# Optimization experiments

Hardware: AMD Instinct MI355X
Metric: run time of the kernel (lower is better)

## Reference

```python
import jax, jax.numpy as jnp
import numpy as np

D_MODEL = 256
NHEAD = 8
HEAD_DIM = D_MODEL // NHEAD
NUM_BOND_TYPES = 5
SCALE = float(np.sqrt(HEAD_DIM))


def setup_inputs() -> dict:
    key = jax.random.key(0)
    ks = jax.random.split(key, 12)
    B, N = 8, 1024
    s = 1.0 / np.sqrt(D_MODEL)
    x = jax.random.normal(ks[0], (B, N, D_MODEL), dtype=jnp.float32)
    adj_matrix = jax.random.randint(ks[1], (B, N, N), 0, NUM_BOND_TYPES, dtype=jnp.int32)
    Wq = jax.random.uniform(ks[2], (D_MODEL, D_MODEL), jnp.float32, -s, s)
    bq = jax.random.uniform(ks[3], (D_MODEL,), jnp.float32, -s, s)
    Wk = jax.random.uniform(ks[4], (D_MODEL, D_MODEL), jnp.float32, -s, s)
    bk = jax.random.uniform(ks[5], (D_MODEL,), jnp.float32, -s, s)
    Wv = jax.random.uniform(ks[6], (D_MODEL, D_MODEL), jnp.float32, -s, s)
    bv = jax.random.uniform(ks[7], (D_MODEL,), jnp.float32, -s, s)
    Wo = jax.random.uniform(ks[8], (D_MODEL, D_MODEL), jnp.float32, -s, s)
    bo = jax.random.uniform(ks[9], (D_MODEL,), jnp.float32, -s, s)
    # edge bias table (num_bond_types, nhead); torch init is zeros, use small randn so it matters
    edge_emb = 0.02 * jax.random.normal(ks[10], (NUM_BOND_TYPES, NHEAD), dtype=jnp.float32)
    return {"x": x, "adj_matrix": adj_matrix, "Wq": Wq, "bq": bq, "Wk": Wk, "bk": bk,
            "Wv": Wv, "bv": bv, "Wo": Wo, "bo": bo, "edge_emb": edge_emb}


def reference(x, adj_matrix, Wq, bq, Wk, bk, Wv, bv, Wo, bo, edge_emb):
    B, N, _ = x.shape
    # projections -> (B, H, N, Dh)
    def proj(W, b):
        return (x @ W.T + b).reshape(B, N, NHEAD, HEAD_DIM).transpose(0, 2, 1, 3)
    Q = proj(Wq, bq)
    K = proj(Wk, bk)
    V = proj(Wv, bv)
    scores = jnp.einsum('bhqd,bhkd->bhqk', Q, K) / SCALE  # (B,H,N,N)
    bias = edge_emb[adj_matrix]                            # (B,N,N,H)
    scores = scores + bias.transpose(0, 3, 1, 2)
    attn = jax.nn.softmax(scores, axis=-1)                 # dropout p=0 (eval) -> identity
    out = jnp.einsum('bhqk,bhkd->bhqd', attn, V)
    out = out.transpose(0, 2, 1, 3).reshape(B, N, D_MODEL)
    return out @ Wo.T + bo
```

## Files before the change

kernel.cpp:

```cpp
#include <hip/hip_runtime.h>
#include <hip/hip_bf16.h>

typedef float f32x4 __attribute__((ext_vector_type(4)));
typedef float f32x16 __attribute__((ext_vector_type(16)));
typedef __bf16 bf16x8 __attribute__((ext_vector_type(8)));
typedef unsigned int uint2v __attribute__((ext_vector_type(2)));

#define MFMA16(a, b, c) __builtin_amdgcn_mfma_f32_16x16x32_bf16((a), (b), (c), 0, 0, 0)
#define MFMA32(a, b, c) __builtin_amdgcn_mfma_f32_32x32x16_bf16((a), (b), (c), 0, 0, 0)

static __device__ __forceinline__ short f2s(float f) {
    __hip_bfloat16 h = __float2bfloat16(f);
    return *reinterpret_cast<short*>(&h);
}
static __device__ __forceinline__ unsigned int cvtpk(float lo, float hi) {
    unsigned int r;
    asm("v_cvt_pk_bf16_f32 %0, %1, %2" : "=v"(r) : "v"(lo), "v"(hi));
    return r;
}
static __device__ __forceinline__ float exp2f_fast(float x) {
#if __has_builtin(__builtin_amdgcn_exp2f)
    return __builtin_amdgcn_exp2f(x);
#else
    return exp2f(x);
#endif
}

__global__ __launch_bounds__(256)
void qkv3_and_gather(const float* __restrict__ x,
                     const float* __restrict__ Wq, const float* __restrict__ bq,
                     const float* __restrict__ Wk, const float* __restrict__ bk,
                     const float* __restrict__ Wv, const float* __restrict__ bv,
                     short* __restrict__ Qb, short* __restrict__ Kb, short* __restrict__ Vb,
                     const int* __restrict__ adj, unsigned int* __restrict__ adjG)
{
    __shared__ short As[128 * 72];
    __shared__ short Bs[3][64 * 72];

    const int bx = blockIdx.x;
    const int tid = threadIdx.x;

    if (bx < 256) {
        const int lane = tid & 63;
        const int wid = tid >> 6;
        const int wr = wid >> 1, wc = wid & 1;
        const int g = lane >> 4, li = lane & 15;

        const int m0 = (bx & 63) * 128;
        const int wc0 = (bx >> 6) * 64;

        const float* Wm[3]  = { Wq, Wk, Wv };
        const float* bm[3]  = { bq, bk, bv };
        short*       Om[3]  = { Qb, Kb, Vb };

        f32x4 acc[3][4][2] = {};

        const int sr = tid >> 4;
        const int sc4 = (tid & 15) * 4;

        for (int k0 = 0; k0 < 256; k0 += 64) {
            __syncthreads();
#pragma unroll
            for (int it = 0; it < 8; ++it) {
                int row = sr + it * 16;
                float4 v = *reinterpret_cast<const float4*>(&x[(m0 + row) * 256 + k0 + sc4]);
                short4 s4;
                s4.x = f2s(v.x); s4.y = f2s(v.y); s4.z = f2s(v.z); s4.w = f2s(v.w);
                *reinterpret_cast<short4*>(&As[row * 72 + sc4]) = s4;
            }
#pragma unroll
            for (int mat = 0; mat < 3; ++mat) {
#pragma unroll
                for (int it = 0; it < 4; ++it) {
                    int row = sr + it * 16;
                    float4 v = *reinterpret_cast<const float4*>(
                        &Wm[mat][(wc0 + row) * 256 + k0 + sc4]);
                    short4 s4;
                    s4.x = f2s(v.x); s4.y = f2s(v.y); s4.z = f2s(v.z); s4.w = f2s(v.w);
                    *reinterpret_cast<short4*>(&Bs[mat][row * 72 + sc4]) = s4;
                }
            }
            __syncthreads();
#pragma unroll
            for (int ks = 0; ks < 2; ++ks) {
                const int kb = ks * 32 + g * 8;
                bf16x8 a[4];
#pragma unroll
                for (int i = 0; i < 4; ++i)
                    a[i] = *reinterpret_cast<const bf16x8*>(&As[(wr * 64 + i * 16 + li) * 72 + kb]);
#pragma unroll
                for (int mat = 0; mat < 3; ++mat) {
                    bf16x8 bfr[2];
#pragma unroll
                    for (int j = 0; j < 2; ++j)
                        bfr[j] = *reinterpret_cast<const bf16x8*>(
                            &Bs[mat][(wc * 32 + j * 16 + li) * 72 + kb]);
#pragma unroll
                    for (int i = 0; i < 4; ++i)
#pragma unroll
                        for (int j = 0; j < 2; ++j)
                            acc[mat][i][j] = MFMA16(a[i], bfr[j], acc[mat][i][j]);
                }
            }
        }

#pragma unroll
        for (int mat = 0; mat < 3; ++mat) {
#pragma unroll
            for (int j = 0; j < 2; ++j) {
                const int colW = wc0 + wc * 32 + j * 16 + li;
                const int h = colW >> 5, d = colW & 31;
                const float bv_ = bm[mat][colW];
#pragma unroll
                for (int i = 0; i < 4; ++i) {
#pragma unroll
                    for (int r = 0; r < 4; ++r) {
                        const int row = m0 + wr * 64 + i * 16 + g * 4 + r;
                        const int bb = row >> 10, nq = row & 1023;
                        Om[mat][((bb * 8 + h) * 1024 + nq) * 32 + d] =
                            f2s(acc[mat][i][j][r] + bv_);
                    }
                }
            }
        }
    } else {
        const int gx = bx - 256;
        const int qt = gx & 31;
        const int b  = (gx >> 5) & 7;
        const int j0 = (gx >> 8) * 8;

        const int4* base = reinterpret_cast<const int4*>(
            adj + ((size_t)(b * 1024 + qt * 32)) * 1024);
        unsigned int* outT = adjG + ((size_t)(b * 32 + qt)) * 16 * 512;

        const int t = tid >> 4;
        const int i = (tid >> 1) & 7;
        const int laneb = 32 * (tid & 1);

#pragma unroll
        for (int jj = 0; jj < 8; ++jj) {
            const int j = j0 + jj;
            const int4 c = base[j * 256 + tid];
            const unsigned int packed =
                (unsigned)c.x | ((unsigned)c.y << 8) | ((unsigned)c.z << 16) | ((unsigned)c.w << 24);
            outT[t * 512 + i * 64 + (j + laneb)] = packed;
        }
    }
}

__global__ __launch_bounds__(256, 2)
void attn11(const short* __restrict__ Qb, const short* __restrict__ Kb,
            const short* __restrict__ Vb, const unsigned int* __restrict__ adjG,
            const float* __restrict__ edge_emb, short* __restrict__ AO)
{
    __shared__ __align__(16) short Ks[4][64 * 36];
    __shared__ __align__(16) short Vt[4][32 * 72];
    __shared__ float Etab[8];

    const int tid = threadIdx.x, lane = tid & 63, wid = tid >> 6;
    const int l5 = lane & 31, h32 = lane >> 5;

    const int orig = blockIdx.x + blockIdx.y * 8;
    const int flat = (orig & 7) * 64 + (orig >> 3);
    const int qb = flat & 7, bh = flat >> 3;
    const int b = bh >> 3, h = bh & 7;
    const int qt = qb * 4 + wid;
    const int q  = qt * 32 + l5;

    const short* Qh = Qb + bh * (1024 * 32);
    const short* Kh = Kb + bh * (1024 * 32);
    const short* Vh = Vb + bh * (1024 * 32);
    const unsigned int* adjT = adjG + ((size_t)(b * 32 + qt)) * 16 * 512;

    if (tid < 5) Etab[tid] = __expf(edge_emb[tid * 8 + h]);

    const bf16x8 qf0 = *reinterpret_cast<const bf16x8*>(&Qh[q * 32 + h32 * 8]);
    const bf16x8 qf1 = *reinterpret_cast<const bf16x8*>(&Qh[q * 32 + 16 + h32 * 8]);

    const float c1 = 0.25503486f;
    const f32x16 zero16 = {};

    f32x16 o[2] = {};
    float lr[2] = { 0.f, 0.f };

    const int sr = tid >> 2;
    const int sc = (tid & 3) * 8;
    const int srh = sr >> 3, srl = sr & 7;
    const int scg2 = (sc >> 3) << 1;

#pragma unroll
    for (int par = 0; par < 2; ++par) {
        const int row = par * 64 + sr;
        int4 kr = *reinterpret_cast<const int4*>(&Kh[row * 32 + sc]);
        int4 vr = *reinterpret_cast<const int4*>(&Vh[row * 32 + sc]);
        short* kd = &Ks[par][sr * 36 + sc];
        *reinterpret_cast<short4*>(kd)     = *reinterpret_cast<short4*>(&kr);
        *reinterpret_cast<short4*>(kd + 4) = *(reinterpret_cast<short4*>(&kr) + 1);
        const short* vs = reinterpret_cast<const short*>(&vr);
#pragma unroll
        for (int i = 0; i < 8; ++i) {
            const int swz = srh ^ i ^ scg2;
            Vt[par][(sc + i) * 72 + swz * 8 + srl] = vs[i];
        }
    }
    __syncthreads();

    for (int p = 0; p < 8; ++p) {
        const int cur = (p & 1) * 2;

        unsigned int a4[2][8];
#pragma unroll
        for (int par = 0; par < 2; ++par)
#pragma unroll
            for (int i = 0; i < 8; ++i)
                a4[par][i] = adjT[(2 * p + par) * 512 + i * 64 + lane];

        int4 kn[2], vn[2];
        if (p < 7) {
#pragma unroll
            for (int par = 0; par < 2; ++par) {
                const int row = (p + 1) * 128 + par * 64 + sr;
                kn[par] = *reinterpret_cast<const int4*>(&Kh[row * 32 + sc]);
                vn[par] = *reinterpret_cast<const int4*>(&Vh[row * 32 + sc]);
            }
        }

        f32x16 s[2][2];
#pragma unroll
        for (int par = 0; par < 2; ++par)
#pragma unroll
            for (int ks = 0; ks < 2; ++ks) {
                union { short4 h4[2]; bf16x8 v; } kfa, kfb;
                const int rowb = (ks * 32 + l5) * 36;
                const short* KsC = &Ks[cur + par][0];
                kfa.h4[0] = *reinterpret_cast<const short4*>(&KsC[rowb + h32 * 8]);
                kfa.h4[1] = *reinterpret_cast<const short4*>(&KsC[rowb + h32 * 8 + 4]);
                kfb.h4[0] = *reinterpret_cast<const short4*>(&KsC[rowb + 16 + h32 * 8]);
                kfb.h4[1] = *reinterpret_cast<const short4*>(&KsC[rowb + 16 + h32 * 8 + 4]);
                s[par][ks] = MFMA32(kfa.v, qf0, zero16);
                s[par][ks] = MFMA32(kfb.v, qf1, s[par][ks]);
            }

        unsigned int pw[2][2][8];
#pragma unroll
        for (int par = 0; par < 2; ++par) {
            float lsum = 0.f;
#pragma unroll
            for (int ks = 0; ks < 2; ++ks) {
#pragma unroll
                for (int rg = 0; rg < 4; ++rg) {
                    const unsigned int aw4 = a4[par][ks * 4 + rg] << 2;
                    float pv[4];
#pragma unroll
                    for (int j = 0; j < 4; ++j) {
                        const float Ev = *reinterpret_cast<const float*>(
                            reinterpret_cast<const char*>(&Etab[0]) +
                            ((aw4 >> (8 * j)) & 0x3FCu));
                        const float pe = exp2f_fast(s[par][ks][rg * 4 + j] * c1);
                        const float pp = pe * Ev;
                        pv[j] = pp;
                        lsum += pp;
                    }
                    pw[par][ks][rg * 2 + 0] = cvtpk(pv[0], pv[1]);
                    pw[par][ks][rg * 2 + 1] = cvtpk(pv[2], pv[3]);
                }
            }
            lr[par] += lsum;
        }

#pragma unroll
        for (int par = 0; par < 2; ++par)
#pragma unroll
            for (int kc = 0; kc < 4; ++kc) {
                const int ks = kc >> 1, half = kc & 1;
                const unsigned int A0 = pw[par][ks][4 * half + 0], A1 = pw[par][ks][4 * half + 1];
                const unsigned int B0 = pw[par][ks][4 * half + 2], B1 = pw[par][ks][4 * half + 3];
                union { unsigned int u[4]; bf16x8 v; } P;
#if __has_builtin(__builtin_amdgcn_permlane32_swap)
                uint2v r02 = __builtin_amdgcn_permlane32_swap(A0, B0, false, false);
                uint2v r13 = __builtin_amdgcn_permlane32_swap(A1, B1, false, false);
                P.u[0] = r02.x; P.u[1] = r13.x;
                P.u[2] = r02.y; P.u[3] = r13.y;
#else
                const unsigned int send0 = h32 ? A0 : B0, send1 = h32 ? A1 : B1;
                const unsigned int rv0 = __shfl_xor(send0, 32);
                const unsigned int rv1 = __shfl_xor(send1, 32);
                const unsigned int own0 = h32 ? B0 : A0, own1 = h32 ? B1 : A1;
                P.u[0] = h32 ? rv0 : own0;
                P.u[1] = h32 ? rv1 : own1;
                P.u[2] = h32 ? own0 : rv0;
                P.u[3] = h32 ? own1 : rv1;
#endif
                const int swzr = (kc * 2 + h32) ^ (l5 & 7) ^ ((l5 >> 3) << 1);
                bf16x8 vf = *reinterpret_cast<const bf16x8*>(
                    &Vt[cur + par][l5 * 72 + swzr * 8]);
                o[par] = MFMA32(vf, P.v, o[par]);
            }

        if (p < 7) {
#pragma unroll
            for (int par = 0; par < 2; ++par) {
                short* kd = &Ks[(cur ^ 2) + par][sr * 36 + sc];
                *reinterpret_cast<short4*>(kd)     = *reinterpret_cast<short4*>(&kn[par]);
                *reinterpret_cast<short4*>(kd + 4) = *(reinterpret_cast<short4*>(&kn[par]) + 1);
                const short* vs = reinterpret_cast<const short*>(&vn[par]);
#pragma unroll
                for (int i = 0; i < 8; ++i) {
                    const int swz = srh ^ i ^ scg2;
                    Vt[(cur ^ 2) + par][(sc + i) * 72 + swz * 8 + srl] = vs[i];
                }
            }
            __syncthreads();
        }
    }

    float lsum = lr[0] + lr[1];
    lsum += __shfl_xor(lsum, 32);
    const float inv = 1.0f / lsum;
    short* dst = &AO[((size_t)(b * 1024 + q)) * 256 + h * 32];
#pragma unroll
    for (int rg = 0; rg < 4; ++rg) {
        short4 s4;
        s4.x = f2s((o[0][rg * 4 + 0] + o[1][rg * 4 + 0]) * inv);
        s4.y = f2s((o[0][rg * 4 + 1] + o[1][rg * 4 + 1]) * inv);
        s4.z = f2s((o[0][rg * 4 + 2] + o[1][rg * 4 + 2]) * inv);
        s4.w = f2s((o[0][rg * 4 + 3] + o[1][rg * 4 + 3]) * inv);
        *reinterpret_cast<short4*>(&dst[rg * 8 + h32 * 4]) = s4;
    }
}

__global__ __launch_bounds__(256)
void out_gemm(const short* __restrict__ AO, const float* __restrict__ Wo,
              const float* __restrict__ bo, float* __restrict__ out)
{
    __shared__ short As[128 * 72];
    __shared__ short Bs[64 * 72];

    const int tid = threadIdx.x, lane = tid & 63, wid = tid >> 6;
    const int wr = wid >> 1, wcn = wid & 1;
    const int g = lane >> 4, li = lane & 15;
    const int m0 = blockIdx.x * 128, n0 = blockIdx.y * 64;

    f32x4 acc[4][2] = {};
    const int ar = tid >> 3, ac8 = (tid & 7) * 8;
    const int br = tid >> 4, bc4 = (tid & 15) * 4;

    for (int k0 = 0; k0 < 256; k0 += 64) {
        __syncthreads();
#pragma unroll
        for (int it = 0; it < 4; ++it) {
            int row = ar + it * 32;
            *reinterpret_cast<int4*>(&As[row * 72 + ac8]) =
                *reinterpret_cast<const int4*>(&AO[(m0 + row) * 256 + k0 + ac8]);
        }
#pragma unroll
        for (int it = 0; it < 4; ++it) {
            int row = br + it * 16;
            float4 v = *reinterpret_cast<const float4*>(&Wo[(n0 + row) * 256 + k0 + bc4]);
            short4 s4; s4.x = f2s(v.x); s4.y = f2s(v.y); s4.z = f2s(v.z); s4.w = f2s(v.w);
            *reinterpret_cast<short4*>(&Bs[row * 72 + bc4]) = s4;
        }
        __syncthreads();
#pragma unroll
        for (int ks = 0; ks < 2; ++ks) {
            const int kb = ks * 32 + g * 8;
            bf16x8 a[4], bb[2];
#pragma unroll
            for (int i = 0; i < 4; ++i)
                a[i] = *reinterpret_cast<const bf16x8*>(&As[(wr * 64 + i * 16 + li) * 72 + kb]);
#pragma unroll
            for (int j = 0; j < 2; ++j)
                bb[j] = *reinterpret_cast<const bf16x8*>(&Bs[(wcn * 32 + j * 16 + li) * 72 + kb]);
#pragma unroll
            for (int i = 0; i < 4; ++i)
#pragma unroll
                for (int j = 0; j < 2; ++j)
                    acc[i][j] = MFMA16(a[i], bb[j], acc[i][j]);
        }
    }
#pragma unroll
    for (int j = 0; j < 2; ++j) {
        const int col = n0 + wcn * 32 + j * 16 + li;
        const float bv_ = bo[col];
#pragma unroll
        for (int i = 0; i < 4; ++i)
#pragma unroll
            for (int r = 0; r < 4; ++r) {
                const int row = m0 + wr * 64 + i * 16 + g * 4 + r;
                out[row * 256 + col] = acc[i][j][r] + bv_;
            }
    }
}

extern "C" void kernel_launch(void* const* d_in, const int* in_sizes, int n_in,
                              void* d_out, int out_size, void* d_ws, size_t ws_size,
                              hipStream_t stream)
{
    const float* x  = (const float*)d_in[0];
    const int*   adj = (const int*)d_in[1];
    const float* Wq = (const float*)d_in[2];
    const float* bq = (const float*)d_in[3];
    const float* Wk = (const float*)d_in[4];
    const float* bk = (const float*)d_in[5];
    const float* Wv = (const float*)d_in[6];
    const float* bv = (const float*)d_in[7];
    const float* Wo = (const float*)d_in[8];
    const float* bo = (const float*)d_in[9];
    const float* ee = (const float*)d_in[10];
    float* out = (float*)d_out;

    short* Qb = (short*)d_ws;
    short* Kb = Qb + 2 * 1024 * 1024;
    short* Vb = Kb + 2 * 1024 * 1024;
    short* AO = Vb + 2 * 1024 * 1024;
    unsigned int* adjG = (unsigned int*)(AO + 2 * 1024 * 1024);

    qkv3_and_gather<<<1280, 256, 0, stream>>>(x, Wq, bq, Wk, bk, Wv, bv,
                                              Qb, Kb, Vb, adj, adjG);
    attn11<<<dim3(8, 64), 256, 0, stream>>>(Qb, Kb, Vb, adjG, ee, AO);
    out_gemm<<<dim3(64, 4), 256, 0, stream>>>(AO, Wo, bo, out);
}
```

Baseline: 52.22 us.

## Split attention key range across warp pairs and double the grid

The attention kernel now assigns two query tiles per block instead of four. Each tile's 1024 keys are split between two warps, each walking half the key range, and the partial outputs and row sums are merged through shared memory at the end. The grid doubles to 1024 blocks and the launch bound asks for 4 blocks per CU to raise occupancy and parallelism. In exchange, K/V tiles are staged per key-half, so each block reuses them across fewer query tiles, and the final reduction adds an extra sync and a shared-memory round trip.

```diff
diff --git a/kernel.cpp b/kernel.cpp
--- a/kernel.cpp
+++ b/kernel.cpp
@@ -148,8 +148,8 @@
     }
 }
 
-__global__ __launch_bounds__(256, 2)
-void attn11(const short* __restrict__ Qb, const short* __restrict__ Kb,
+__global__ __launch_bounds__(256, 4)
+void attn12(const short* __restrict__ Qb, const short* __restrict__ Kb,
             const short* __restrict__ Vb, const unsigned int* __restrict__ adjG,
             const float* __restrict__ edge_emb, short* __restrict__ AO)
 {
@@ -159,12 +159,13 @@
 
     const int tid = threadIdx.x, lane = tid & 63, wid = tid >> 6;
     const int l5 = lane & 31, h32 = lane >> 5;
-
-    const int orig = blockIdx.x + blockIdx.y * 8;
-    const int flat = (orig & 7) * 64 + (orig >> 3);
-    const int qb = flat & 7, bh = flat >> 3;
+    const int qw = wid & 1, kh = wid >> 1;
+
+    const int orig = blockIdx.x + blockIdx.y * 16;
+    const int flat = (orig & 7) * 128 + (orig >> 3);
+    const int qb = flat & 15, bh = flat >> 4;
     const int b = bh >> 3, h = bh & 7;
-    const int qt = qb * 4 + wid;
+    const int qt = qb * 2 + qw;
     const int q  = qt * 32 + l5;
 
     const short* Qh = Qb + bh * (1024 * 32);
@@ -180,8 +181,8 @@
     const float c1 = 0.25503486f;
     const f32x16 zero16 = {};
 
-    f32x16 o[2] = {};
-    float lr[2] = { 0.f, 0.f };
+    f32x16 o = {};
+    float lr = 0.f;
 
     const int sr = tid >> 2;
     const int sc = (tid & 3) * 8;
@@ -189,143 +190,147 @@
     const int scg2 = (sc >> 3) << 1;
 
 #pragma unroll
-    for (int par = 0; par < 2; ++par) {
-        const int row = par * 64 + sr;
+    for (int u = 0; u < 2; ++u) {
+        const int row = u * 512 + sr;
         int4 kr = *reinterpret_cast<const int4*>(&Kh[row * 32 + sc]);
         int4 vr = *reinterpret_cast<const int4*>(&Vh[row * 32 + sc]);
-        short* kd = &Ks[par][sr * 36 + sc];
+        short* kd = &Ks[u][sr * 36 + sc];
         *reinterpret_cast<short4*>(kd)     = *reinterpret_cast<short4*>(&kr);
         *reinterpret_cast<short4*>(kd + 4) = *(reinterpret_cast<short4*>(&kr) + 1);
         const short* vs = reinterpret_cast<const short*>(&vr);
 #pragma unroll
         for (int i = 0; i < 8; ++i) {
             const int swz = srh ^ i ^ scg2;
-            Vt[par][(sc + i) * 72 + swz * 8 + srl] = vs[i];
+            Vt[u][(sc + i) * 72 + swz * 8 + srl] = vs[i];
         }
     }
     __syncthreads();
 
-    for (int p = 0; p < 8; ++p) {
-        const int cur = (p & 1) * 2;
-
-        unsigned int a4[2][8];
-#pragma unroll
-        for (int par = 0; par < 2; ++par)
-#pragma unroll
-            for (int i = 0; i < 8; ++i)
-                a4[par][i] = adjT[(2 * p + par) * 512 + i * 64 + lane];
+    for (int t = 0; t < 8; ++t) {
+        const int cur = (t & 1) * 2;
+        const int tt = kh * 8 + t;
+
+        unsigned int a4[8];
+#pragma unroll
+        for (int i = 0; i < 8; ++i)
+            a4[i] = adjT[tt * 512 + i * 64 + lane];
 
         int4 kn[2], vn[2];
-        if (p < 7) {
-#pragma unroll
-            for (int par = 0; par < 2; ++par) {
-                const int row = (p + 1) * 128 + par * 64 + sr;
-                kn[par] = *reinterpret_cast<const int4*>(&Kh[row * 32 + sc]);
-                vn[par] = *reinterpret_cast<const int4*>(&Vh[row * 32 + sc]);
-            }
-        }
-
-        f32x16 s[2][2];
-#pragma unroll
-        for (int par = 0; par < 2; ++par)
+        if (t < 7) {
+#pragma unroll
+            for (int u = 0; u < 2; ++u) {
+                const int row = u * 512 + (t + 1) * 64 + sr;
+                kn[u] = *reinterpret_cast<const int4*>(&Kh[row * 32 + sc]);
+                vn[u] = *reinterpret_cast<const int4*>(&Vh[row * 32 + sc]);
+            }
+        }
+
+        f32x16 s[2];
+        {
+            const short* KsC = &Ks[cur + kh][0];
 #pragma unroll
             for (int ks = 0; ks < 2; ++ks) {
                 union { short4 h4[2]; bf16x8 v; } kfa, kfb;
                 const int rowb = (ks * 32 + l5) * 36;
-                const short* KsC = &Ks[cur + par][0];
                 kfa.h4[0] = *reinterpret_cast<const short4*>(&KsC[rowb + h32 * 8]);
                 kfa.h4[1] = *reinterpret_cast<const short4*>(&KsC[rowb + h32 * 8 + 4]);
                 kfb.h4[0] = *reinterpret_cast<const short4*>(&KsC[rowb + 16 + h32 * 8]);
                 kfb.h4[1] = *reinterpret_cast<const short4*>(&KsC[rowb + 16 + h32 * 8 + 4]);
-                s[par][ks] = MFMA32(kfa.v, qf0, zero16);
-                s[par][ks] = MFMA32(kfb.v, qf1, s[par][ks]);
-            }
-
-        unsigned int pw[2][2][8];
-#pragma unroll
-        for (int par = 0; par < 2; ++par) {
-            float lsum = 0.f;
-#pragma unroll
-            for (int ks = 0; ks < 2; ++ks) {
-#pragma unroll
-                for (int rg = 0; rg < 4; ++rg) {
-                    const unsigned int aw4 = a4[par][ks * 4 + rg] << 2;
-                    float pv[4];
-#pragma unroll
-                    for (int j = 0; j < 4; ++j) {
-                        const float Ev = *reinterpret_cast<const float*>(
-                            reinterpret_cast<const char*>(&Etab[0]) +
-                            ((aw4 >> (8 * j)) & 0x3FCu));
-                        const float pe = exp2f_fast(s[par][ks][rg * 4 + j] * c1);
-                        const float pp = pe * Ev;
-                        pv[j] = pp;
-                        lsum += pp;
-                    }
-                    pw[par][ks][rg * 2 + 0] = cvtpk(pv[0], pv[1]);
-                    pw[par][ks][rg * 2 + 1] = cvtpk(pv[2], pv[3]);
+                s[ks] = MFMA32(kfa.v, qf0, zero16);
+                s[ks] = MFMA32(kfb.v, qf1, s[ks]);
+            }
+        }
+
+        unsigned int pw[2][8];
+#pragma unroll
+        for (int ks = 0; ks < 2; ++ks) {
+#pragma unroll
+            for (int rg = 0; rg < 4; ++rg) {
+                const unsigned int aw4 = a4[ks * 4 + rg] << 2;
+                float pv[4];
+#pragma unroll
+                for (int j = 0; j < 4; ++j) {
+                    const float Ev = *reinterpret_cast<const float*>(
+                        reinterpret_cast<const char*>(&Etab[0]) +
+                        ((aw4 >> (8 * j)) & 0x3FCu));
+                    const float pe = exp2f_fast(s[ks][rg * 4 + j] * c1);
+                    const float pp = pe * Ev;
+                    pv[j] = pp;
+                    lr += pp;
                 }
-            }
-            lr[par] += lsum;
-        }
-
-#pragma unroll
-        for (int par = 0; par < 2; ++par)
-#pragma unroll
-            for (int kc = 0; kc < 4; ++kc) {
-                const int ks = kc >> 1, half = kc & 1;
-                const unsigned int A0 = pw[par][ks][4 * half + 0], A1 = pw[par][ks][4 * half + 1];
-                const unsigned int B0 = pw[par][ks][4 * half + 2], B1 = pw[par][ks][4 * half + 3];
-                union { unsigned int u[4]; bf16x8 v; } P;
+                pw[ks][rg * 2 + 0] = cvtpk(pv[0], pv[1]);
+                pw[ks][rg * 2 + 1] = cvtpk(pv[2], pv[3]);
+            }
+        }
+
+#pragma unroll
+        for (int kc = 0; kc < 4; ++kc) {
+            const int ks = kc >> 1, half = kc & 1;
+            const unsigned int A0 = pw[ks][4 * half + 0], A1 = pw[ks][4 * half + 1];
+            const unsigned int B0 = pw[ks][4 * half + 2], B1 = pw[ks][4 * half + 3];
+            union { unsigned int u[4]; bf16x8 v; } P;
 #if __has_builtin(__builtin_amdgcn_permlane32_swap)
-                uint2v r02 = __builtin_amdgcn_permlane32_swap(A0, B0, false, false);
-                uint2v r13 = __builtin_amdgcn_permlane32_swap(A1, B1, false, false);
-                P.u[0] = r02.x; P.u[1] = r13.x;
-                P.u[2] = r02.y; P.u[3] = r13.y;
+            uint2v r02 = __builtin_amdgcn_permlane32_swap(A0, B0, false, false);
+            uint2v r13 = __builtin_amdgcn_permlane32_swap(A1, B1, false, false);
+            P.u[0] = r02.x; P.u[1] = r13.x;
+            P.u[2] = r02.y; P.u[3] = r13.y;
 #else
-                const unsigned int send0 = h32 ? A0 : B0, send1 = h32 ? A1 : B1;
-                const unsigned int rv0 = __shfl_xor(send0, 32);
-                const unsigned int rv1 = __shfl_xor(send1, 32);
-                const unsigned int own0 = h32 ? B0 : A0, own1 = h32 ? B1 : A1;
-                P.u[0] = h32 ? rv0 : own0;
-                P.u[1] = h32 ? rv1 : own1;
-                P.u[2] = h32 ? own0 : rv0;
-                P.u[3] = h32 ? own1 : rv1;
+            const unsigned int send0 = h32 ? A0 : B0, send1 = h32 ? A1 : B1;
+            const unsigned int rv0 = __shfl_xor(send0, 32);
+            const unsigned int rv1 = __shfl_xor(send1, 32);
+            const unsigned int own0 = h32 ? B0 : A0, own1 = h32 ? B1 : A1;
+            P.u[0] = h32 ? rv0 : own0;
+            P.u[1] = h32 ? rv1 : own1;
+            P.u[2] = h32 ? own0 : rv0;
+            P.u[3] = h32 ? own1 : rv1;
 #endif
-                const int swzr = (kc * 2 + h32) ^ (l5 & 7) ^ ((l5 >> 3) << 1);
-                bf16x8 vf = *reinterpret_cast<const bf16x8*>(
-                    &Vt[cur + par][l5 * 72 + swzr * 8]);
-                o[par] = MFMA32(vf, P.v, o[par]);
-            }
-
-        if (p < 7) {
-#pragma unroll
-            for (int par = 0; par < 2; ++par) {
-                short* kd = &Ks[(cur ^ 2) + par][sr * 36 + sc];
-                *reinterpret_cast<short4*>(kd)     = *reinterpret_cast<short4*>(&kn[par]);
-                *reinterpret_cast<short4*>(kd + 4) = *(reinterpret_cast<short4*>(&kn[par]) + 1);
-                const short* vs = reinterpret_cast<const short*>(&vn[par]);
+            const int swzr = (kc * 2 + h32) ^ (l5 & 7) ^ ((l5 >> 3) << 1);
+            bf16x8 vf = *reinterpret_cast<const bf16x8*>(
+                &Vt[cur + kh][l5 * 72 + swzr * 8]);
+            o = MFMA32(vf, P.v, o);
+        }
+
+        if (t < 7) {
+#pragma unroll
+            for (int u = 0; u < 2; ++u) {
+                short* kd = &Ks[(cur ^ 2) + u][sr * 36 + sc];
+                *reinterpret_cast<short4*>(kd)     = *reinterpret_cast<short4*>(&kn[u]);
+                *reinterpret_cast<short4*>(kd + 4) = *(reinterpret_cast<short4*>(&kn[u]) + 1);
+                const short* vs = reinterpret_cast<const short*>(&vn[u]);
 #pragma unroll
                 for (int i = 0; i < 8; ++i) {
                     const int swz = srh ^ i ^ scg2;
-                    Vt[(cur ^ 2) + par][(sc + i) * 72 + swz * 8 + srl] = vs[i];
+                    Vt[(cur ^ 2) + u][(sc + i) * 72 + swz * 8 + srl] = vs[i];
                 }
             }
             __syncthreads();
         }
     }
 
-    float lsum = lr[0] + lr[1];
-    lsum += __shfl_xor(lsum, 32);
-    const float inv = 1.0f / lsum;
-    short* dst = &AO[((size_t)(b * 1024 + q)) * 256 + h * 32];
-#pragma unroll
-    for (int rg = 0; rg < 4; ++rg) {
-        short4 s4;
-        s4.x = f2s((o[0][rg * 4 + 0] + o[1][rg * 4 + 0]) * inv);
-        s4.y = f2s((o[0][rg * 4 + 1] + o[1][rg * 4 + 1]) * inv);
-        s4.z = f2s((o[0][rg * 4 + 2] + o[1][rg * 4 + 2]) * inv);
-        s4.w = f2s((o[0][rg * 4 + 3] + o[1][rg * 4 + 3]) * inv);
-        *reinterpret_cast<short4*>(&dst[rg * 8 + h32 * 4]) = s4;
+    float* scr = reinterpret_cast<float*>(&Ks[0][0]);
+    if (kh == 1) {
+        float* myb = scr + qw * 1152 + lane * 18;
+        myb[0] = lr;
+#pragma unroll
+        for (int r = 0; r < 16; ++r) myb[1 + r] = o[r];
+    }
+    __syncthreads();
+
+    if (kh == 0) {
+        const float* pb = scr + qw * 1152 + lane * 18;
+        float lsum = lr + pb[0];
+        lsum += __shfl_xor(lsum, 32);
+        const float inv = 1.0f / lsum;
+        short* dst = &AO[((size_t)(b * 1024 + q)) * 256 + h * 32];
+#pragma unroll
+        for (int rg = 0; rg < 4; ++rg) {
+            short4 s4;
+            s4.x = f2s((o[rg * 4 + 0] + pb[1 + rg * 4 + 0]) * inv);
+            s4.y = f2s((o[rg * 4 + 1] + pb[1 + rg * 4 + 1]) * inv);
+            s4.z = f2s((o[rg * 4 + 2] + pb[1 + rg * 4 + 2]) * inv);
+            s4.w = f2s((o[rg * 4 + 3] + pb[1 + rg * 4 + 3]) * inv);
+            *reinterpret_cast<short4*>(&dst[rg * 8 + h32 * 4]) = s4;
+        }
     }
 }
 
@@ -417,6 +422,6 @@
 
     qkv3_and_gather<<<1280, 256, 0, stream>>>(x, Wq, bq, Wk, bk, Wv, bv,
                                               Qb, Kb, Vb, adj, adjG);
-    attn11<<<dim3(8, 64), 256, 0, stream>>>(Qb, Kb, Vb, adjG, ee, AO);
+    attn12<<<dim3(16, 64), 256, 0, stream>>>(Qb, Kb, Vb, adjG, ee, AO);
     out_gemm<<<dim3(64, 4), 256, 0, stream>>>(AO, Wo, bo, out);
 }
```

Result: no change. 52.63 us (+0.8%).
